# Performance work log

Hardware: AMD Instinct MI355X
Metric: run time of the kernel (lower is better)

The kernel has to match this reference:

```python
import jax, jax.numpy as jnp
import numpy as np

N_NODES = 50000
N_EDGES = 800000
N_GRAPHS = 64
PIP = 3
N_CLASSES = 10
EPS = 1e-5


def setup_inputs() -> dict:
    key = jax.random.key(0)
    ks = jax.random.split(key, 32)
    s = 0.05
    d = {}
    d["node_feats"] = jax.random.normal(ks[0], (N_NODES, 128), jnp.float32)
    d["edge_w"] = jax.random.uniform(ks[1], (N_EDGES,), jnp.float32)
    # stacked per-branch params
    d["conv_w"] = jax.random.normal(ks[2], (PIP, 96, 128, 3), jnp.float32) * s
    d["conv_b"] = jax.random.normal(ks[3], (PIP, 96), jnp.float32) * s
    d["gcn_w"] = jax.random.normal(ks[4], (PIP, 96, 54), jnp.float32) * s
    d["gcn_b"] = jax.random.normal(ks[5], (PIP, 54), jnp.float32) * s
    d["bn1_g"] = jnp.ones((96,), jnp.float32)
    d["bn1_b"] = jnp.zeros((96,), jnp.float32)
    d["bn2_g"] = jnp.ones((54,), jnp.float32)
    d["bn2_b"] = jnp.zeros((54,), jnp.float32)
    d["bn3_g"] = jnp.ones((75,), jnp.float32)
    d["bn3_b"] = jnp.zeros((75,), jnp.float32)
    d["press_w"] = jax.random.normal(ks[6], (1, PIP, PIP), jnp.float32) * s
    d["press_b"] = jax.random.normal(ks[7], (1,), jnp.float32) * s
    d["jk_w1"] = jax.random.normal(ks[8], (54, 34), jnp.float32) * s
    d["jk_b1"] = jax.random.normal(ks[9], (34,), jnp.float32) * s
    d["jk_w2"] = jax.random.normal(ks[10], (34, 25), jnp.float32) * s
    d["jk_b2"] = jax.random.normal(ks[11], (25,), jnp.float32) * s
    d["jk_w3"] = jax.random.normal(ks[12], (25, 16), jnp.float32) * s
    d["jk_b3"] = jax.random.normal(ks[13], (16,), jnp.float32) * s
    d["cls1_w"] = jax.random.normal(ks[14], (75, 120), jnp.float32) * s
    d["cls1_b"] = jax.random.normal(ks[15], (120,), jnp.float32) * s
    d["cls2_w"] = jax.random.normal(ks[16], (120, N_CLASSES), jnp.float32) * s
    d["cls2_b"] = jax.random.normal(ks[17], (N_CLASSES,), jnp.float32) * s
    d["edge_src"] = jax.random.randint(ks[18], (N_EDGES,), 0, N_NODES)
    d["edge_dst"] = jax.random.randint(ks[19], (N_EDGES,), 0, N_NODES)
    d["graph_ids"] = jnp.sort(jax.random.randint(ks[20], (N_NODES,), 0, N_GRAPHS))
    return d


def _bn(x, g, b):
    # training-mode BatchNorm1d over axis 0
    m = x.mean(0)
    v = x.var(0)
    return g * (x - m) * jax.lax.rsqrt(v + EPS) + b


def _gconv(h, W, b, src, dst, ew, n):
    # DGL GraphConv norm='none': sum_{(u,v)} w_e * h[u] -> @W + b
    msg = h[src] * ew[:, None]              # [E, F]
    agg = jax.ops.segment_sum(msg, dst, num_segments=n)  # [N, F]
    return agg @ W + b


def _dconv1d(x, w, b, dil):
    # x: [1, Cin, N], w: [Cout, Cin, K]; 'same' length via pad=dil for K=3
    out = jax.lax.conv_general_dilated(
        x, w, window_strides=(1,), padding=[(dil, dil)],
        rhs_dilation=(dil,), dimension_numbers=('NCH', 'OIH', 'NCH'))
    return out + b[None, :, None]


def reference(node_feats, edge_w, conv_w, conv_b, gcn_w, gcn_b,
              bn1_g, bn1_b, bn2_g, bn2_b, bn3_g, bn3_b,
              press_w, press_b, jk_w1, jk_b1, jk_w2, jk_b2, jk_w3, jk_b3,
              cls1_w, cls1_b, cls2_w, cls2_b,
              edge_src, edge_dst, graph_ids):
    n = node_feats.shape[0]
    relu = jax.nn.relu
    # ---- BN_embedding ----
    h0 = node_feats.T[None]                # [1, 128, N]
    h0x = [_dconv1d(h0, conv_w[i], conv_b[i], i + 1) for i in range(PIP)]
    h2x = []
    for i in range(PIP):
        a = h0x[i % PIP][0].T              # [N, 96]
        c = h0x[(i + 1) % PIP][0].T        # [N, 96]
        h1 = _bn(relu(a) + c, bn1_g, bn1_b)          # cross_connect
        t = _gconv(h1, gcn_w[i], gcn_b[i], edge_src, edge_dst, edge_w, n)
        h2x.append(relu(t))                # [N, 54]
    stacked = jnp.stack(h2x, axis=1)       # [N, PIP, 54]
    pressed = jax.lax.conv_general_dilated(
        stacked, press_w, window_strides=(1,), padding='SAME',
        dimension_numbers=('NCH', 'OIH', 'NCH')) + press_b[None, :, None]
    emd_h = _bn(pressed[:, 0, :], bn2_g, bn2_b)      # [N, 54] (dropout = identity, eval)
    # ---- Presentation (JK readout) ----
    h1 = relu(_gconv(emd_h, jk_w1, jk_b1, edge_src, edge_dst, edge_w, n))
    h2 = relu(_gconv(h1, jk_w2, jk_b2, edge_src, edge_dst, edge_w, n))
    h3 = relu(_gconv(h2, jk_w3, jk_b3, edge_src, edge_dst, edge_w, n))
    ac_h = jnp.concatenate([h1, h2, h3], axis=1)     # [N, 75]
    hg = jax.ops.segment_sum(ac_h, graph_ids, num_segments=N_GRAPHS)  # [B, 75]
    logits = _bn(hg, bn3_g, bn3_b) @ cls1_w + cls1_b
    logits = logits @ cls2_w + cls2_b
    return (logits, emd_h)
```

## Files before the change

kernel.cpp:

```cpp
#include <hip/hip_runtime.h>
#include <hip/hip_bf16.h>

#define NND 50000
#define NED 800000
#define NGR 64
#define EPSV 1e-5f
#define NSTR (NND + 8)

__global__ void hist_kernel(const int* __restrict__ dst, int* __restrict__ cnt)
{
    int e = blockIdx.x * 256 + threadIdx.x;
    if (e < NED) atomicAdd(&cnt[dst[e]], 1);
}

__global__ void scanA_kernel(const int* __restrict__ cnt, int* __restrict__ bsum)
{
    __shared__ int buf[256];
    int t = threadIdx.x, base = blockIdx.x * 1024;
    int s = 0;
    for (int i = t; i < 1024; i += 256) {
        int idx = base + i;
        s += (idx < NND) ? cnt[idx] : 0;
    }
    buf[t] = s; __syncthreads();
    for (int off = 128; off; off >>= 1) {
        if (t < off) buf[t] += buf[t + off];
        __syncthreads();
    }
    if (t == 0) bsum[blockIdx.x] = buf[0];
}

__global__ void scanB_kernel(int* __restrict__ bsum, int* __restrict__ rowptr, int nb)
{
    if (threadIdx.x == 0) {
        int acc = 0;
        for (int i = 0; i < nb; i++) { int v = bsum[i]; bsum[i] = acc; acc += v; }
        rowptr[NND] = acc;
    }
}

__global__ void scanC_kernel(const int* __restrict__ cnt, const int* __restrict__ bsum,
                             int* __restrict__ rowptr, int* __restrict__ cursor)
{
    __shared__ int buf[1024];
    int t = threadIdx.x, idx = blockIdx.x * 1024 + t;
    int v = (idx < NND) ? cnt[idx] : 0;
    buf[t] = v; __syncthreads();
    for (int off = 1; off < 1024; off <<= 1) {
        int x = (t >= off) ? buf[t - off] : 0;
        __syncthreads();
        buf[t] += x;
        __syncthreads();
    }
    if (idx < NND) {
        int excl = buf[t] - v + bsum[blockIdx.x];
        rowptr[idx] = excl; cursor[idx] = excl;
    }
}

__global__ void fill_kernel(const int* __restrict__ src, const int* __restrict__ dst,
                            const float* __restrict__ ew, int* __restrict__ cursor,
                            int* __restrict__ csrs, float* __restrict__ csrw)
{
    int e = blockIdx.x * 256 + threadIdx.x;
    if (e < NED) {
        int pos = atomicAdd(&cursor[dst[e]], 1);
        csrs[pos] = src[e];
        csrw[pos] = ew[e];
    }
}

__global__ void grstart_kernel(const int* __restrict__ gid, int* __restrict__ gr)
{
    int t = threadIdx.x;
    if (t > NGR) return;
    if (t == NGR) { gr[NGR] = NND; return; }
    int lo = 0, hi = NND;
    while (lo < hi) { int mid = (lo + hi) >> 1; if (gid[mid] < t) lo = mid + 1; else hi = mid; }
    gr[t] = lo;
}

__global__ void transpose_kernel(const float* __restrict__ nf, float* __restrict__ nfT)
{
    __shared__ float tile[32][33];
    int tx = threadIdx.x & 31, ty = threadIdx.x >> 5;
    int p0 = blockIdx.x * 32, c0 = blockIdx.y * 32;
#pragma unroll
    for (int i = 0; i < 4; i++) {
        int p = p0 + ty + i * 8;
        if (p < NND) tile[ty + i * 8][tx] = nf[(size_t)p * 128 + c0 + tx];
    }
    __syncthreads();
#pragma unroll
    for (int i = 0; i < 4; i++) {
        int c = c0 + ty + i * 8;
        int p = p0 + tx;
        if (p < NND) nfT[(size_t)c * NSTR + 4 + p] = tile[tx][ty + i * 8];
    }
}

__global__ void pad_kernel(float* __restrict__ nfT)
{
    int t = threadIdx.x;
    int c = t >> 3, i = t & 7;
    size_t off = (size_t)c * NSTR + (i < 4 ? i : (NND + i));
    nfT[off] = 0.f;
}

template <int D>
__device__ __forceinline__ void conv_tap4(const float4& lo, const float4& mi, const float4& hi,
                                          const float* __restrict__ wl, int c,
                                          float (&acc)[4][4])
{
    float f0[4], f1[4], f2[4];
    f1[0] = mi.x; f1[1] = mi.y; f1[2] = mi.z; f1[3] = mi.w;
    if (D == 1) {
        f0[0] = lo.w; f0[1] = mi.x; f0[2] = mi.y; f0[3] = mi.z;
        f2[0] = mi.y; f2[1] = mi.z; f2[2] = mi.w; f2[3] = hi.x;
    } else if (D == 2) {
        f0[0] = lo.z; f0[1] = lo.w; f0[2] = mi.x; f0[3] = mi.y;
        f2[0] = mi.z; f2[1] = mi.w; f2[2] = hi.x; f2[3] = hi.y;
    } else {
        f0[0] = lo.y; f0[1] = lo.z; f0[2] = lo.w; f0[3] = mi.x;
        f2[0] = mi.w; f2[1] = hi.x; f2[2] = hi.y; f2[3] = hi.z;
    }
    const int BR = D - 1;
    const float4 a0 = *(const float4*)&wl[((BR * 3 + 0) * 128 + c) * 4];
    const float4 a1 = *(const float4*)&wl[((BR * 3 + 1) * 128 + c) * 4];
    const float4 a2 = *(const float4*)&wl[((BR * 3 + 2) * 128 + c) * 4];
#pragma unroll
    for (int i = 0; i < 4; i++) {
        acc[0][i] += f0[i] * a0.x + f1[i] * a1.x + f2[i] * a2.x;
        acc[1][i] += f0[i] * a0.y + f1[i] * a1.y + f2[i] * a2.y;
        acc[2][i] += f0[i] * a0.z + f1[i] * a1.z + f2[i] * a2.z;
        acc[3][i] += f0[i] * a0.w + f1[i] * a1.w + f2[i] * a2.w;
    }
}

__global__ __launch_bounds__(256)
void conv_y_stats_kernel(const float* __restrict__ nfT, const float* __restrict__ cw,
                         const float* __restrict__ cb, float* __restrict__ Y,
                         float* __restrict__ st1)
{
    __shared__ __align__(16) float wl[3 * 3 * 128 * 4];
    const int t  = threadIdx.x;
    const int og = blockIdx.x;
    for (int l = t; l < 3 * 3 * 128 * 4; l += 256) {
        int j = l & 3; int c = (l >> 2) & 127; int kb = l >> 9;
        int k = kb % 3, br = kb / 3;
        wl[l] = cw[(((size_t)br * 96 + og * 4 + j) * 128 + c) * 3 + k];
    }
    __syncthreads();
    const int pq = blockIdx.y * 1024 + t * 4;
    float acc[3][4][4];
#pragma unroll
    for (int br = 0; br < 3; br++)
#pragma unroll
        for (int j = 0; j < 4; j++) {
            float b = cb[br * 96 + og * 4 + j];
#pragma unroll
            for (int i = 0; i < 4; i++) acc[br][j][i] = b;
        }
    for (int c = 0; c < 128; c++) {
        const float* col = nfT + (size_t)c * NSTR + 4;
        float4 lo = *(const float4*)(col + pq - 4);
        float4 mi = *(const float4*)(col + pq);
        float4 hi = *(const float4*)(col + pq + 4);
        conv_tap4<1>(lo, mi, hi, wl, c, acc[0]);
        conv_tap4<2>(lo, mi, hi, wl, c, acc[1]);
        conv_tap4<3>(lo, mi, hi, wl, c, acc[2]);
    }
#pragma unroll
    for (int j = 0; j < 4; j++)
#pragma unroll
        for (int i = 0; i < 4; i++) {
            float a0 = acc[0][j][i], a1 = acc[1][j][i], a2 = acc[2][j][i];
            acc[0][j][i] = (a0 > 0.f ? a0 : 0.f) + a1;
            acc[1][j][i] = (a1 > 0.f ? a1 : 0.f) + a2;
            acc[2][j][i] = (a2 > 0.f ? a2 : 0.f) + a0;
        }
    bool val[4];
#pragma unroll
    for (int i = 0; i < 4; i++) val[i] = (pq + i) < NND;
    const size_t NM = (size_t)NND * 96;
#pragma unroll
    for (int br = 0; br < 3; br++)
#pragma unroll
        for (int j = 0; j < 4; j++) {
            float s = 0.f, q = 0.f;
#pragma unroll
            for (int i = 0; i < 4; i++)
                if (val[i]) { float v = acc[br][j][i]; s += v; q += v * v; }
            for (int off = 32; off; off >>= 1) {
                s += __shfl_down(s, off, 64);
                q += __shfl_down(q, off, 64);
            }
            if ((t & 63) == 0) {
                unsafeAtomicAdd(&st1[br * 96 + og * 4 + j], s);
                unsafeAtomicAdd(&st1[288 + br * 96 + og * 4 + j], q);
            }
        }
#pragma unroll
    for (int br = 0; br < 3; br++)
#pragma unroll
        for (int i = 0; i < 4; i++) {
            if (!val[i]) continue;
            float* yo = Y + (size_t)br * NM + (size_t)(pq + i) * 96 + og * 4;
            float4 v;
            v.x = acc[br][0][i]; v.y = acc[br][1][i]; v.z = acc[br][2][i]; v.w = acc[br][3][i];
            *(float4*)yo = v;
        }
}

__global__ void bn_finalize_kernel(const float* __restrict__ st, const float* __restrict__ g,
                                   const float* __restrict__ b,
                                   float* __restrict__ sc, float* __restrict__ sh,
                                   int C, int gmod)
{
    int t = threadIdx.x;
    if (t >= C) return;
    float mean = st[t] / (float)NND;
    float var  = st[C + t] / (float)NND - mean * mean;
    float rs = rsqrtf(var + EPSV);
    float gg = g[t % gmod], bb = b[t % gmod];
    float s = gg * rs;
    sc[t] = s; sh[t] = bb - mean * s;
}

__global__ void fold_w_kernel(const float* __restrict__ gw, const float* __restrict__ sc1,
                              const float* __restrict__ sh1,
                              float* __restrict__ WP, float* __restrict__ BP)
{
    int t = blockIdx.x * 256 + threadIdx.x;
    if (t >= 3 * 54) return;
    int br = t / 54, o = t % 54;
    const float* W = gw + (size_t)br * 96 * 54 + o;
    float bacc = 0.f;
    for (int c = 0; c < 96; c++) {
        float w = W[c * 54];
        WP[((size_t)br * 96 + c) * 54 + o] = sc1[br * 96 + c] * w;
        bacc += sh1[br * 96 + c] * w;
    }
    BP[br * 54 + o] = bacc;
}

template <int Cin, int Cout, bool RELU>
__global__ __launch_bounds__(128)
void matmul_node_kernel(const float* __restrict__ in, const float* __restrict__ W,
                        const float* __restrict__ bias, float* __restrict__ out)
{
    constexpr int CoutP = (Cout + 3) & ~3;
    __shared__ __align__(16) float wl[Cin * CoutP];
    __shared__ float bl[CoutP];
    const int t = threadIdx.x;
    const int br = blockIdx.y;
    const float* Wb = W + (size_t)br * Cin * Cout;
    for (int l = t; l < Cin * CoutP; l += 128) {
        int c = l / CoutP, o = l % CoutP;
        wl[l] = (o < Cout) ? Wb[c * Cout + o] : 0.f;
    }
    if (t < CoutP) bl[t] = (t < Cout && bias) ? bias[br * Cout + t] : 0.f;
    __syncthreads();
    int p = blockIdx.x * 128 + t;
    if (p >= NND) return;
    float acc[CoutP];
#pragma unroll
    for (int o = 0; o < CoutP; o++) acc[o] = bl[o];
    const float* row = in + (size_t)br * NND * Cin + (size_t)p * Cin;
    if constexpr (Cin % 4 == 0) {
        const float4* row4 = (const float4*)row;
#pragma unroll
        for (int c4 = 0; c4 < Cin / 4; c4++) {
            float4 f4 = row4[c4];
            float fv[4] = {f4.x, f4.y, f4.z, f4.w};
#pragma unroll
            for (int cc = 0; cc < 4; cc++) {
                const float4* w4 = (const float4*)&wl[(c4 * 4 + cc) * CoutP];
#pragma unroll
                for (int oq = 0; oq < CoutP / 4; oq++) {
                    float4 wv = w4[oq];
                    acc[oq * 4 + 0] += fv[cc] * wv.x;
                    acc[oq * 4 + 1] += fv[cc] * wv.y;
                    acc[oq * 4 + 2] += fv[cc] * wv.z;
                    acc[oq * 4 + 3] += fv[cc] * wv.w;
                }
            }
        }
    } else if constexpr (Cin % 2 == 0) {
        const float2* row2 = (const float2*)row;
#pragma unroll
        for (int c2 = 0; c2 < Cin / 2; c2++) {
            float2 f2 = row2[c2];
            float fv[2] = {f2.x, f2.y};
#pragma unroll
            for (int cc = 0; cc < 2; cc++) {
                const float4* w4 = (const float4*)&wl[(c2 * 2 + cc) * CoutP];
#pragma unroll
                for (int oq = 0; oq < CoutP / 4; oq++) {
                    float4 wv = w4[oq];
                    acc[oq * 4 + 0] += fv[cc] * wv.x;
                    acc[oq * 4 + 1] += fv[cc] * wv.y;
                    acc[oq * 4 + 2] += fv[cc] * wv.z;
                    acc[oq * 4 + 3] += fv[cc] * wv.w;
                }
            }
        }
    } else {
#pragma unroll
        for (int c = 0; c < Cin; c++) {
            float f = row[c];
            const float4* w4 = (const float4*)&wl[c * CoutP];
#pragma unroll
            for (int oq = 0; oq < CoutP / 4; oq++) {
                float4 wv = w4[oq];
                acc[oq * 4 + 0] += f * wv.x;
                acc[oq * 4 + 1] += f * wv.y;
                acc[oq * 4 + 2] += f * wv.z;
                acc[oq * 4 + 3] += f * wv.w;
            }
        }
    }
    float* op = out + (size_t)br * NND * Cout + (size_t)p * Cout;
#pragma unroll
    for (int o = 0; o < Cout; o++) {
        float v = acc[o];
        if constexpr (RELU) v = v > 0.f ? v : 0.f;
        op[o] = v;
    }
}

__global__ void pull3br54_kernel(const float* __restrict__ Z, const int* __restrict__ rowptr,
                                 const int* __restrict__ csrs, const float* __restrict__ csrw,
                                 const float* __restrict__ gb, float* __restrict__ H2c)
{
    int id = blockIdx.x * 256 + threadIdx.x;
    if (id >= NND * 27) return;
    int p = id / 27, q = id % 27;
    const float2* Z2 = (const float2*)Z;
    const size_t NQ = (size_t)NND * 27;
    int beg = rowptr[p], end = rowptr[p + 1];
    float a0x=0,a0y=0, a1x=0,a1y=0, a2x=0,a2y=0;
    for (int i = beg; i < end; i++) {
        float w = csrw[i];
        size_t off = (size_t)csrs[i] * 27 + q;
        float2 v0 = Z2[off];
        float2 v1 = Z2[NQ + off];
        float2 v2 = Z2[2 * NQ + off];
        a0x += w * v0.x; a0y += w * v0.y;
        a1x += w * v1.x; a1y += w * v1.y;
        a2x += w * v2.x; a2y += w * v2.y;
    }
    const float2* GB2 = (const float2*)gb;
    float2* O2 = (float2*)H2c;
    size_t ob = (size_t)p * 27 + q;
    {
        float2 b = GB2[q], r;
        r.x = a0x + b.x; r.y = a0y + b.y;
        r.x = r.x > 0.f ? r.x : 0.f; r.y = r.y > 0.f ? r.y : 0.f;
        O2[ob] = r;
    }
    {
        float2 b = GB2[27 + q], r;
        r.x = a1x + b.x; r.y = a1y + b.y;
        r.x = r.x > 0.f ? r.x : 0.f; r.y = r.y > 0.f ? r.y : 0.f;
        O2[NQ + ob] = r;
    }
    {
        float2 b = GB2[54 + q], r;
        r.x = a2x + b.x; r.y = a2y + b.y;
        r.x = r.x > 0.f ? r.x : 0.f; r.y = r.y > 0.f ? r.y : 0.f;
        O2[2 * NQ + ob] = r;
    }
}

template <int C>
__global__ void pull_br2_kernel(const float* __restrict__ in, const int* __restrict__ rowptr,
                                const int* __restrict__ csrs, const float* __restrict__ csrw,
                                const float* __restrict__ bias, float* __restrict__ out)
{
    constexpr int C2 = C / 2;
    int id = blockIdx.x * 256 + threadIdx.x;
    if (id >= NND * C2) return;
    int p = id / C2, q = id % C2;
    const float2* in2 = (const float2*)in;
    int beg = rowptr[p], end = rowptr[p + 1];
    float ax = 0.f, ay = 0.f;
    for (int i = beg; i < end; i++) {
        float w = csrw[i];
        float2 v = in2[(size_t)csrs[i] * C2 + q];
        ax += w * v.x; ay += w * v.y;
    }
    float2 b = ((const float2*)bias)[q];
    float2 r;
    r.x = ax + b.x; r.y = ay + b.y;
    r.x = r.x > 0.f ? r.x : 0.f; r.y = r.y > 0.f ? r.y : 0.f;
    ((float2*)out)[(size_t)p * C2 + q] = r;
}

template <int C>
__global__ void pull_br1_kernel(const float* __restrict__ in, const int* __restrict__ rowptr,
                                const int* __restrict__ csrs, const float* __restrict__ csrw,
                                const float* __restrict__ bias, float* __restrict__ out)
{
    int id = blockIdx.x * 256 + threadIdx.x;
    if (id >= NND * C) return;
    int p = id / C, c = id % C;
    int beg = rowptr[p], end = rowptr[p + 1];
    float acc = 0.f;
    for (int i = beg; i < end; i++)
        acc += csrw[i] * in[(size_t)csrs[i] * C + c];
    float v = acc + bias[c];
    out[id] = v > 0.f ? v : 0.f;
}

template <int C>
__global__ void pull_br4_kernel(const float* __restrict__ in, const int* __restrict__ rowptr,
                                const int* __restrict__ csrs, const float* __restrict__ csrw,
                                const float* __restrict__ bias, float* __restrict__ out)
{
    constexpr int C4 = C / 4;
    int id = blockIdx.x * 256 + threadIdx.x;
    if (id >= NND * C4) return;
    int p = id / C4, q = id % C4;
    const float4* in4 = (const float4*)in;
    int beg = rowptr[p], end = rowptr[p + 1];
    float ax = 0.f, ay = 0.f, az = 0.f, aw = 0.f;
    for (int i = beg; i < end; i++) {
        float w = csrw[i];
        float4 v = in4[(size_t)csrs[i] * C4 + q];
        ax += w * v.x; ay += w * v.y; az += w * v.z; aw += w * v.w;
    }
    float4 b = ((const float4*)bias)[q];
    float4 r;
    r.x = ax + b.x; r.y = ay + b.y; r.z = az + b.z; r.w = aw + b.w;
    r.x = r.x > 0.f ? r.x : 0.f; r.y = r.y > 0.f ? r.y : 0.f;
    r.z = r.z > 0.f ? r.z : 0.f; r.w = r.w > 0.f ? r.w : 0.f;
    ((float4*)out)[(size_t)p * C4 + q] = r;
}

__global__ void press_stats_kernel(const float* __restrict__ H2, const float* __restrict__ pw,
                                   const float* __restrict__ pb, float* __restrict__ PRS,
                                   float* __restrict__ st2)
{
    __shared__ float ls[54], lq[54];
    int t = threadIdx.x;
    if (t < 54) { ls[t] = 0.f; lq[t] = 0.f; }
    __syncthreads();
    float pwf[9];
#pragma unroll
    for (int q = 0; q < 9; q++) pwf[q] = pw[q];
    float pbf = pb[0];
    const size_t NM = (size_t)NND * 54;
    size_t base = (size_t)blockIdx.x * 6912;
    for (int q = 0; q < 27; q++) {
        size_t idx = base + q * 256 + t;
        if (idx < NM) {
            int p = (int)(idx / 54), h = (int)(idx % 54);
            float sum = pbf;
#pragma unroll
            for (int i = 0; i < 3; i++)
#pragma unroll
                for (int k = 0; k < 3; k++) {
                    int hh = h + k - 1;
                    if (hh >= 0 && hh < 54)
                        sum += pwf[i * 3 + k] * H2[(size_t)i * NM + (size_t)p * 54 + hh];
                }
            PRS[idx] = sum;
            atomicAdd(&ls[h], sum); atomicAdd(&lq[h], sum * sum);
        }
    }
    __syncthreads();
    if (t < 54) {
        unsafeAtomicAdd(&st2[t], ls[t]);
        unsafeAtomicAdd(&st2[54 + t], lq[t]);
    }
}

__global__ void emd_kernel(float* __restrict__ PRS, const float* __restrict__ sc2,
                           const float* __restrict__ sh2, float* __restrict__ outp)
{
    int id = blockIdx.x * 256 + threadIdx.x;
    if (id >= NND * 54) return;
    int h = id % 54;
    float v = PRS[id] * sc2[h] + sh2[h];
    PRS[id] = v;
    outp[id] = v;
}

__global__ void pool_kernel(const float* __restrict__ H1, const float* __restrict__ H2j,
                            const float* __restrict__ H3, const int* __restrict__ gr,
                            float* __restrict__ HG)
{
    __shared__ float part[4][75];
    int t = threadIdx.x;
    int c = t % 75, sub = t / 75;
    int g = blockIdx.x;
    int s = gr[g], e = gr[g + 1];
    float acc = 0.f;
    for (int p = s + sub; p < e; p += 4) {
        float v;
        if (c < 34)      v = H1[(size_t)p * 34 + c];
        else if (c < 59) v = H2j[(size_t)p * 25 + (c - 34)];
        else             v = H3[(size_t)p * 16 + (c - 59)];
        acc += v;
    }
    part[sub][c] = acc;
    __syncthreads();
    if (t < 75) HG[g * 75 + t] = part[0][t] + part[1][t] + part[2][t] + part[3][t];
}

__global__ void final_kernel(const float* __restrict__ HG, const float* __restrict__ g3,
                             const float* __restrict__ b3,
                             const float* __restrict__ w1, const float* __restrict__ b1,
                             const float* __restrict__ w2, const float* __restrict__ b2,
                             float* __restrict__ outp)
{
    __shared__ float hg[64 * 75];
    __shared__ float o1[64 * 120];
    __shared__ float sc[75], sh[75];
    int t = threadIdx.x;
    for (int idx = t; idx < 64 * 75; idx += 512) hg[idx] = HG[idx];
    __syncthreads();
    if (t < 75) {
        float s = 0.f, q = 0.f;
        for (int r = 0; r < 64; r++) { float v = hg[r * 75 + t]; s += v; q += v * v; }
        float m = s / 64.f, var = q / 64.f - m * m;
        float rs = rsqrtf(var + EPSV);
        float scale = g3[t] * rs;
        sc[t] = scale; sh[t] = b3[t] - m * scale;
    }
    __syncthreads();
    for (int idx = t; idx < 64 * 75; idx += 512) { int c = idx % 75; hg[idx] = hg[idx] * sc[c] + sh[c]; }
    __syncthreads();
    for (int idx = t; idx < 64 * 120; idx += 512) {
        int r = idx / 120, o = idx % 120;
        float a = b1[o];
        for (int c = 0; c < 75; c++) a += hg[r * 75 + c] * w1[c * 120 + o];
        o1[idx] = a;
    }
    __syncthreads();
    for (int idx = t; idx < 640; idx += 512) {
        int r = idx / 10, o = idx % 10;
        float a = b2[o];
        for (int k = 0; k < 120; k++) a += o1[r * 120 + k] * w2[k * 10 + o];
        outp[idx] = a;
    }
}

extern "C" void kernel_launch(void* const* d_in, const int* in_sizes, int n_in,
                              void* d_out, int out_size, void* d_ws, size_t ws_size,
                              hipStream_t stream)
{
    (void)in_sizes; (void)n_in; (void)out_size;
    const float* nf     = (const float*)d_in[0];
    const float* ew     = (const float*)d_in[1];
    const float* conv_w = (const float*)d_in[2];
    const float* conv_b = (const float*)d_in[3];
    const float* gcn_w  = (const float*)d_in[4];
    const float* gcn_b  = (const float*)d_in[5];
    const float* bn1_g = (const float*)d_in[6],  *bn1_b = (const float*)d_in[7];
    const float* bn2_g = (const float*)d_in[8],  *bn2_b = (const float*)d_in[9];
    const float* bn3_g = (const float*)d_in[10], *bn3_b = (const float*)d_in[11];
    const float* press_w = (const float*)d_in[12], *press_b = (const float*)d_in[13];
    const float* jk_w1 = (const float*)d_in[14], *jk_b1 = (const float*)d_in[15];
    const float* jk_w2 = (const float*)d_in[16], *jk_b2 = (const float*)d_in[17];
    const float* jk_w3 = (const float*)d_in[18], *jk_b3 = (const float*)d_in[19];
    const float* cls1_w = (const float*)d_in[20], *cls1_b = (const float*)d_in[21];
    const float* cls2_w = (const float*)d_in[22], *cls2_b = (const float*)d_in[23];
    const int* esrc = (const int*)d_in[24];
    const int* edst = (const int*)d_in[25];
    const int* gid  = (const int*)d_in[26];
    float* out = (float*)d_out;

    float* ws = (float*)d_ws;
    const size_t NM = (size_t)NND * 96;
    const size_t N54 = (size_t)NND * 54;
    float* X   = ws;
    float* Y   = X + 3 * NM;
    float* H2c = Y + 3 * NM;
    float* PRS = H2c + 3 * N54;
    float* ST1 = PRS + N54;
    float* SC1 = ST1 + 576;
    float* SH1 = SC1 + 288;
    float* ST2 = SH1 + 288;
    float* SC2 = ST2 + 108;
    float* SH2 = SC2 + 54;
    float* HG  = SH2 + 54;
    int* CNT    = (int*)(HG + 4800);
    int* ROWPTR = CNT + NND;
    int* CURSOR = ROWPTR + NND + 1;
    int* CSRS   = CURSOR + NND;
    float* CSRW = (float*)(CSRS + NED);
    int* BSUM   = (int*)(CSRW + NED);
    int* GR     = BSUM + 64;
    float* WP   = (float*)(GR + 68);
    float* BP   = WP + 15552;
    size_t need = (size_t)((BP + 162) - ws) * sizeof(float);
    if (ws_size < need) return;

    float* nfT  = X;
    float* Z    = X;
    float* P1   = Y;
    float* H1j  = P1 + (size_t)NND * 34;
    float* P2   = H1j + (size_t)NND * 34;
    float* H2j  = P2 + (size_t)NND * 25;
    float* P3   = H2j + (size_t)NND * 25;
    float* H3j  = P3 + (size_t)NND * 16;

    hipMemsetAsync(ST1, 0, 1368 * sizeof(float), stream);
    hipMemsetAsync(CNT, 0, NND * sizeof(int), stream);

    hist_kernel<<<(NED + 255) / 256, 256, 0, stream>>>(edst, CNT);
    scanA_kernel<<<49, 256, 0, stream>>>(CNT, BSUM);
    scanB_kernel<<<1, 64, 0, stream>>>(BSUM, ROWPTR, 49);
    scanC_kernel<<<49, 1024, 0, stream>>>(CNT, BSUM, ROWPTR, CURSOR);
    fill_kernel<<<(NED + 255) / 256, 256, 0, stream>>>(esrc, edst, ew, CURSOR, CSRS, CSRW);
    grstart_kernel<<<1, 128, 0, stream>>>(gid, GR);

    transpose_kernel<<<dim3((NND + 31) / 32, 4), 256, 0, stream>>>(nf, nfT);
    pad_kernel<<<1, 1024, 0, stream>>>(nfT);

    conv_y_stats_kernel<<<dim3(24, 49), 256, 0, stream>>>(nfT, conv_w, conv_b, Y, ST1);
    bn_finalize_kernel<<<1, 512, 0, stream>>>(ST1, bn1_g, bn1_b, SC1, SH1, 288, 96);

    fold_w_kernel<<<1, 256, 0, stream>>>(gcn_w, SC1, SH1, WP, BP);
    matmul_node_kernel<96, 54, false><<<dim3((NND + 127) / 128, 3), 128, 0, stream>>>(
        Y, WP, BP, Z);

    pull3br54_kernel<<<(NND * 27 + 255) / 256, 256, 0, stream>>>(
        Z, ROWPTR, CSRS, CSRW, gcn_b, H2c);

    press_stats_kernel<<<(int)((N54 + 6911) / 6912), 256, 0, stream>>>(H2c, press_w, press_b, PRS, ST2);
    bn_finalize_kernel<<<1, 512, 0, stream>>>(ST2, bn2_g, bn2_b, SC2, SH2, 54, 54);
    emd_kernel<<<(int)((N54 + 255) / 256), 256, 0, stream>>>(PRS, SC2, SH2, out + 640);

    matmul_node_kernel<54, 34, false><<<dim3((NND + 127) / 128, 1), 128, 0, stream>>>(
        PRS, jk_w1, nullptr, P1);
    pull_br2_kernel<34><<<(NND * 17 + 255) / 256, 256, 0, stream>>>(
        P1, ROWPTR, CSRS, CSRW, jk_b1, H1j);

    matmul_node_kernel<34, 25, false><<<dim3((NND + 127) / 128, 1), 128, 0, stream>>>(
        H1j, jk_w2, nullptr, P2);
    pull_br1_kernel<25><<<(NND * 25 + 255) / 256, 256, 0, stream>>>(
        P2, ROWPTR, CSRS, CSRW, jk_b2, H2j);

    matmul_node_kernel<25, 16, false><<<dim3((NND + 127) / 128, 1), 128, 0, stream>>>(
        H2j, jk_w3, nullptr, P3);
    pull_br4_kernel<16><<<(NND * 4 + 255) / 256, 256, 0, stream>>>(
        P3, ROWPTR, CSRS, CSRW, jk_b3, H3j);

    pool_kernel<<<NGR, 300, 0, stream>>>(H1j, H2j, H3j, GR, HG);
    final_kernel<<<1, 512, 0, stream>>>(HG, bn3_g, bn3_b, cls1_w, cls1_b, cls2_w, cls2_b, out);
}
```

Baseline: 939.2 us.

## Store conv output in channel-quad-major layout and halve conv block size

The conv kernel now writes Y as [branch][channel-quad][node] float4 planes instead of node-major rows, so consecutive threads write consecutive float4s and stores coalesce. A new matmul kernel reads this layout, with adjacent threads loading adjacent float4s per channel quad rather than striding across 96-float rows. The conv kernel also moves to 128-thread blocks covering 512 nodes each, doubling the grid to improve occupancy and load spread. The now-unused float4 path of the generic matmul is removed.

```diff
diff --git a/kernel.cpp b/kernel.cpp
--- a/kernel.cpp
+++ b/kernel.cpp
@@ -137,7 +137,7 @@
     }
 }
 
-__global__ __launch_bounds__(256)
+__global__ __launch_bounds__(128)
 void conv_y_stats_kernel(const float* __restrict__ nfT, const float* __restrict__ cw,
                          const float* __restrict__ cb, float* __restrict__ Y,
                          float* __restrict__ st1)
@@ -145,13 +145,13 @@
     __shared__ __align__(16) float wl[3 * 3 * 128 * 4];
     const int t  = threadIdx.x;
     const int og = blockIdx.x;
-    for (int l = t; l < 3 * 3 * 128 * 4; l += 256) {
+    for (int l = t; l < 3 * 3 * 128 * 4; l += 128) {
         int j = l & 3; int c = (l >> 2) & 127; int kb = l >> 9;
         int k = kb % 3, br = kb / 3;
         wl[l] = cw[(((size_t)br * 96 + og * 4 + j) * 128 + c) * 3 + k];
     }
     __syncthreads();
-    const int pq = blockIdx.y * 1024 + t * 4;
+    const int pq = blockIdx.y * 512 + t * 4;
     float acc[3][4][4];
 #pragma unroll
     for (int br = 0; br < 3; br++)
@@ -182,7 +182,6 @@
     bool val[4];
 #pragma unroll
     for (int i = 0; i < 4; i++) val[i] = (pq + i) < NND;
-    const size_t NM = (size_t)NND * 96;
 #pragma unroll
     for (int br = 0; br < 3; br++)
 #pragma unroll
@@ -201,15 +200,16 @@
             }
         }
 #pragma unroll
-    for (int br = 0; br < 3; br++)
+    for (int br = 0; br < 3; br++) {
+        float4* yo = (float4*)Y + ((size_t)(br * 24 + og) * NND);
 #pragma unroll
         for (int i = 0; i < 4; i++) {
             if (!val[i]) continue;
-            float* yo = Y + (size_t)br * NM + (size_t)(pq + i) * 96 + og * 4;
             float4 v;
             v.x = acc[br][0][i]; v.y = acc[br][1][i]; v.z = acc[br][2][i]; v.w = acc[br][3][i];
-            *(float4*)yo = v;
-        }
+            yo[pq + i] = v;
+        }
+    }
 }
 
 __global__ void bn_finalize_kernel(const float* __restrict__ st, const float* __restrict__ g,
@@ -244,6 +244,51 @@
     BP[br * 54 + o] = bacc;
 }
 
+template <int Cout>
+__global__ __launch_bounds__(128)
+void matmul_y_kernel(const float* __restrict__ Yq, const float* __restrict__ W,
+                     const float* __restrict__ bias, float* __restrict__ out)
+{
+    constexpr int CoutP = (Cout + 3) & ~3;
+    __shared__ __align__(16) float wl[96 * CoutP];
+    __shared__ float bl[CoutP];
+    const int t = threadIdx.x;
+    const int br = blockIdx.y;
+    const float* Wb = W + (size_t)br * 96 * Cout;
+    for (int l = t; l < 96 * CoutP; l += 128) {
+        int c = l / CoutP, o = l % CoutP;
+        wl[l] = (o < Cout) ? Wb[c * Cout + o] : 0.f;
+    }
+    if (t < CoutP) bl[t] = (t < Cout) ? bias[br * Cout + t] : 0.f;
+    __syncthreads();
+    int p = blockIdx.x * 128 + t;
+    if (p >= NND) return;
+    float acc[CoutP];
+#pragma unroll
+    for (int o = 0; o < CoutP; o++) acc[o] = bl[o];
+    const float4* Y4 = (const float4*)Yq + (size_t)br * 24 * NND;
+#pragma unroll
+    for (int c4 = 0; c4 < 24; c4++) {
+        float4 f4 = Y4[(size_t)c4 * NND + p];
+        float fv[4] = {f4.x, f4.y, f4.z, f4.w};
+#pragma unroll
+        for (int cc = 0; cc < 4; cc++) {
+            const float4* w4 = (const float4*)&wl[(c4 * 4 + cc) * CoutP];
+#pragma unroll
+            for (int oq = 0; oq < CoutP / 4; oq++) {
+                float4 wv = w4[oq];
+                acc[oq * 4 + 0] += fv[cc] * wv.x;
+                acc[oq * 4 + 1] += fv[cc] * wv.y;
+                acc[oq * 4 + 2] += fv[cc] * wv.z;
+                acc[oq * 4 + 3] += fv[cc] * wv.w;
+            }
+        }
+    }
+    float* op = out + (size_t)br * NND * Cout + (size_t)p * Cout;
+#pragma unroll
+    for (int o = 0; o < Cout; o++) op[o] = acc[o];
+}
+
 template <int Cin, int Cout, bool RELU>
 __global__ __launch_bounds__(128)
 void matmul_node_kernel(const float* __restrict__ in, const float* __restrict__ W,
@@ -267,26 +312,7 @@
 #pragma unroll
     for (int o = 0; o < CoutP; o++) acc[o] = bl[o];
     const float* row = in + (size_t)br * NND * Cin + (size_t)p * Cin;
-    if constexpr (Cin % 4 == 0) {
-        const float4* row4 = (const float4*)row;
-#pragma unroll
-        for (int c4 = 0; c4 < Cin / 4; c4++) {
-            float4 f4 = row4[c4];
-            float fv[4] = {f4.x, f4.y, f4.z, f4.w};
-#pragma unroll
-            for (int cc = 0; cc < 4; cc++) {
-                const float4* w4 = (const float4*)&wl[(c4 * 4 + cc) * CoutP];
-#pragma unroll
-                for (int oq = 0; oq < CoutP / 4; oq++) {
-                    float4 wv = w4[oq];
-                    acc[oq * 4 + 0] += fv[cc] * wv.x;
-                    acc[oq * 4 + 1] += fv[cc] * wv.y;
-                    acc[oq * 4 + 2] += fv[cc] * wv.z;
-                    acc[oq * 4 + 3] += fv[cc] * wv.w;
-                }
-            }
-        }
-    } else if constexpr (Cin % 2 == 0) {
+    if constexpr (Cin % 2 == 0) {
         const float2* row2 = (const float2*)row;
 #pragma unroll
         for (int c2 = 0; c2 < Cin / 2; c2++) {
@@ -620,12 +646,11 @@
     transpose_kernel<<<dim3((NND + 31) / 32, 4), 256, 0, stream>>>(nf, nfT);
     pad_kernel<<<1, 1024, 0, stream>>>(nfT);
 
-    conv_y_stats_kernel<<<dim3(24, 49), 256, 0, stream>>>(nfT, conv_w, conv_b, Y, ST1);
+    conv_y_stats_kernel<<<dim3(24, 98), 128, 0, stream>>>(nfT, conv_w, conv_b, Y, ST1);
     bn_finalize_kernel<<<1, 512, 0, stream>>>(ST1, bn1_g, bn1_b, SC1, SH1, 288, 96);
 
     fold_w_kernel<<<1, 256, 0, stream>>>(gcn_w, SC1, SH1, WP, BP);
-    matmul_node_kernel<96, 54, false><<<dim3((NND + 127) / 128, 3), 128, 0, stream>>>(
-        Y, WP, BP, Z);
+    matmul_y_kernel<54><<<dim3((NND + 127) / 128, 3), 128, 0, stream>>>(Y, WP, BP, Z);
 
     pull3br54_kernel<<<(NND * 27 + 255) / 256, 256, 0, stream>>>(
         Z, ROWPTR, CSRS, CSRW, gcn_b, H2c);
```

Result: no change. 942.4 us (+0.3%).
